# Kernel tuning notes

Hardware: AMD Instinct MI355X
Metric: run time of the kernel (lower is better)

Reference implementation:

```python
import jax, jax.numpy as jnp
import numpy as np

# WFN symmetry table: symmetry index -> (px, py, pz) angular-momentum exponents
# (s; px,py,pz; 6 cartesian d; 10 cartesian f) as in standard .wfn files.
WFN_SYMMETRY_INDEX = np.array([
    [0, 0, 0],
    [1, 0, 0], [0, 1, 0], [0, 0, 1],
    [2, 0, 0], [0, 2, 0], [0, 0, 2], [1, 1, 0], [1, 0, 1], [0, 1, 1],
    [3, 0, 0], [0, 3, 0], [0, 0, 3], [2, 1, 0], [2, 0, 1], [0, 2, 1],
    [1, 2, 0], [1, 0, 2], [0, 1, 2], [1, 1, 1],
], dtype=np.float32)


def setup_inputs() -> dict:
    key = jax.random.key(0)
    k1, k2, k3, k4, k5 = jax.random.split(key, 5)
    n, ms, na, nps = 16, 4096, 32, 512
    dv = jax.random.normal(k1, (n, ms, na, 3), jnp.float32)          # sample->atom displacement vectors
    centers = jax.random.randint(k2, (n, nps), 0, na)                # primitive -> atom index (-1 = pad)
    exp = jax.random.uniform(k3, (n, nps), jnp.float32)              # GTO exponents (>0)
    sym = jax.random.randint(k4, (n, nps), 0, 20)                    # symmetry index into WFN table
    dm = jax.random.normal(k5, (n, nps, nps), jnp.float32) / nps     # density matrices
    return {"dv": dv, "centers": centers, "exp": exp, "sym": sym, "dm": dm}


def _density(dv, exp, dm, centers, sym):
    # dv: [n,ms,na,3]; exp: [n,np]; dm: [n,np,np]; centers/sym: [n,np] int
    sym_map = jnp.asarray(WFN_SYMMETRY_INDEX)
    valid = centers >= 0                                   # padded primitives marked -1
    c = jnp.where(valid, centers, 0)
    s = jnp.where(valid, sym, 0)
    r2 = jnp.sum(dv * dv, axis=-1)                         # [n,ms,na] squared distances
    r2g = jax.vmap(lambda r, ci: r[:, ci])(r2, c)          # [n,ms,np] gather per primitive
    dvg = jax.vmap(lambda d, ci: d[:, ci])(dv, c)          # [n,ms,np,3]
    pw = sym_map[s]                                        # [n,np,3] angular exponents
    # GTO kernel: dx^px * dy^py * dz^pz * exp(-alpha * r^2)
    ang = jnp.prod(jnp.power(dvg, pw[:, None, :, :]), axis=-1)   # [n,ms,np]
    basis = ang * jnp.exp(-exp[:, None, :] * r2g)
    basis = basis * valid[:, None, :].astype(basis.dtype)        # zero out padded primitives
    # rho = sum_pq basis_p * dm_pq * basis_q (per molecule, per sample point)
    return jnp.einsum('nmp,npq,nmq->nm', basis, dm, basis)


def reference(dv, centers, exp, sym, dm):
    return _density(dv, exp, dm, centers, sym)
```

## Files before the change

### kernel.cpp

```cpp
#include <hip/hip_runtime.h>
#include <stdint.h>

#define NMOL 16
#define MS   4096
#define NA   32
#define NP   512
#define BM   64
#define TBL  65536u

typedef __attribute__((ext_vector_type(4))) float  f32x4;
typedef __attribute__((ext_vector_type(4))) unsigned int u32x4;
typedef __attribute__((ext_vector_type(2))) unsigned int u32x2;
typedef __attribute__((ext_vector_type(8))) short  s16x8;
typedef unsigned int uint;
typedef unsigned short ushort;

#define WS_DMF_OFF   0u
#define WS_DMF_SZ    (16u*512u*512u*2u)
#define WS_M2A_OFF   (WS_DMF_OFF + WS_DMF_SZ)
#define WS_M2A_SZ    (16u*512u*4u)
#define WS_M2B_OFF   (WS_M2A_OFF + WS_M2A_SZ)
#define WS_M2B_SZ    (16u*512u*4u)
#define WS_ALPH_OFF  (WS_M2B_OFF + WS_M2B_SZ)

__device__ __constant__ uint c_pw[20] = {
  0x000,
  0x001, 0x010, 0x100,
  0x002, 0x020, 0x200, 0x011, 0x101, 0x110,
  0x003, 0x030, 0x300, 0x012, 0x102, 0x120, 0x021, 0x201, 0x210, 0x111
};

__device__ __forceinline__ ushort f2bf(float f) {
  uint u = __float_as_uint(f);
  u = u + 0x7fffu + ((u >> 16) & 1u);
  return (ushort)(u >> 16);
}
__device__ __forceinline__ float bflo(uint u) { return __uint_as_float(u << 16); }
__device__ __forceinline__ float bfhi(uint u) { return __uint_as_float(u & 0xFFFF0000u); }
__device__ __forceinline__ float cvt16lo(uint u) {
  float r; asm("v_cvt_f32_f16 %0, %1" : "=v"(r) : "v"(u)); return r;
}
__device__ __forceinline__ float cvt16hi(uint u) {
  uint s = u >> 16; float r; asm("v_cvt_f32_f16 %0, %1" : "=v"(r) : "v"(s)); return r;
}
__device__ __forceinline__ uint pkmul(uint a, uint b) {
  uint r; asm("v_pk_mul_f16 %0, %1, %2" : "=v"(r) : "v"(a), "v"(b)); return r;
}
__device__ __forceinline__ s16x8 mkfrag(u32x2 lo, u32x2 hi) {
  union { uint u[4]; s16x8 v; } x;
  x.u[0] = lo[0]; x.u[1] = lo[1]; x.u[2] = hi[0]; x.u[3] = hi[1];
  return x.v;
}

__global__ void dm_pack(const float* __restrict__ dm, short* __restrict__ dmF,
                        const int* __restrict__ centers, const int* __restrict__ sym,
                        const float* __restrict__ expg,
                        uint* __restrict__ m2a, uint* __restrict__ m2b,
                        float* __restrict__ alphaS) {
  __shared__ float tile[NP * 16];
  __shared__ float tileT[16 * (NP + 2)];
  const int Q = blockIdx.x, n = blockIdx.y;
  const int t = threadIdx.x;
  const float* base = dm + (size_t)n * NP * NP;
  const float* src  = base + Q * 16;
#pragma unroll
  for (int i = 0; i < 32; ++i) {
    int e = t + 256 * i;
    int p = e >> 4, c = e & 15;
    tile[e] = src[(size_t)p * NP + c];
  }
  const float* srcT = base + (size_t)(Q * 16) * NP;
#pragma unroll
  for (int i = 0; i < 32; ++i) {
    int e = t + 256 * i;
    tileT[(e >> 9) * (NP + 2) + (e & 511)] = srcT[e];
  }
  if (n == 0) {
    int i = Q * 256 + t;
    int craw = centers[i], s = sym[i];
    bool valid = (craw >= 0);
    uint c = (uint)((valid ? craw : 0) & (NA - 1));
    int si = valid ? s : 0;
    si = (si >= 0 && si < 20) ? si : 0;
    uint pw = c_pw[si];
    uint d = (pw & 15u) + ((pw >> 4) & 15u) + ((pw >> 8) & 15u);
    uint h[3]; int k = 0;
#pragma unroll
    for (uint ax = 0; ax < 3; ++ax) {
      uint e = (pw >> (4 * ax)) & 15u;
      for (uint r = 0; r < e; ++r) if (k < 3) h[k++] = c * 512u + ax * 128u;
    }
    while (k < 3) h[k++] = c * 512u;
    m2a[i] = h[0] | (h[1] << 16);
    m2b[i] = h[2] | (d << 14) | (c << 16);
    alphaS[i] = (valid ? -expg[i] : -1e5f) * 1.44269504088896f;
  }
  __syncthreads();
  short* dst = dmF + ((size_t)(n * 32 + Q) * 16) * 512;
#pragma unroll
  for (int i = 0; i < 4; ++i) {
    int v = t + 256 * i;
    int kblk = v >> 6, l = v & 63;
    int p0 = kblk * 32 + ((l >> 4) << 3);
    int col = l & 15;
    int q = Q * 16 + col;
    s16x8 o;
#pragma unroll
    for (int j = 0; j < 8; ++j) {
      int p = p0 + j;
      float w = 0.0f;
      if (p < q)       w = tile[p * 16 + col] + tileT[col * (NP + 2) + p];
      else if (p == q) w = tile[p * 16 + col];
      o[j] = (short)f2bf(w);
    }
    *(s16x8*)(dst + (size_t)v * 8) = o;
  }
}

__launch_bounds__(512, 4)
__global__ void wfn_fused8(const float* __restrict__ dv,
                           const uint* __restrict__ m2aG,
                           const uint* __restrict__ m2bG,
                           const float* __restrict__ alG,
                           const short* __restrict__ dmF,
                           float* __restrict__ out) {
  __shared__ __align__(16) char smem[81920];
  const int t = threadIdx.x;
  const int bid = ((blockIdx.x & 7) << 7) + (blockIdx.x >> 3);
  const int n  = bid >> 6;
  const int m0 = (bid & 63) * BM;

  {
    const float* dvg = dv + (size_t)(n * MS + m0) * (NA * 3);
#pragma unroll
    for (int k = 0; k < 4; ++k) {
      int idx = t + 512 * k;
      int m = idx >> 5, c = idx & 31;
      const float* p = dvg + (m * NA + c) * 3;
      float x = p[0], y = p[1], z = p[2];
      float r2 = fmaf(x, x, fmaf(y, y, z * z));
      uint base = TBL + (uint)c * 512u
                + ((uint)((m >> 3) ^ (c & 7)) << 4) + (uint)((m & 7) << 1);
      *(_Float16*)(smem + base)       = (_Float16)x;
      *(_Float16*)(smem + base + 128) = (_Float16)y;
      *(_Float16*)(smem + base + 256) = (_Float16)z;
      *(_Float16*)(smem + base + 384) = (_Float16)r2;
    }
  }
  __syncthreads();

  {
    const int p = t;
    const uint ma = m2aG[n * NP + p], mb = m2bG[n * NP + p];
    const float al = alG[n * NP + p];
    const uint h0 = ma & 0xFFFFu, h1 = ma >> 16;
    const uint h2 = mb & 0x3FFFu;
    const uint d  = (mb >> 14) & 3u;
    const uint cs = (h0 >> 9) & 7u;
    const uint rh = (h0 & 0xFE00u) + 384u;
    const bool ge2 = (d >= 2), eq3 = (d == 3), eq0 = (d == 0);
    const uint wbase = ((uint)(p >> 5) << 10) + (((uint)(p >> 2) & 1u) << 9)
                     + ((((uint)p & 31u) >> 3) << 7) + (((uint)p & 3u) << 5);
#pragma unroll
    for (int j = 0; j < 8; ++j) {
      uint off = (uint)((j ^ (int)cs) << 4);
      u32x4 qr = *(const u32x4*)(smem + TBL + rh + off);
      u32x4 q0, q1, q2;
      if (!eq0) q0 = *(const u32x4*)(smem + TBL + h0 + off);
      if (ge2)  q1 = *(const u32x4*)(smem + TBL + h1 + off);
      if (eq3)  q2 = *(const u32x4*)(smem + TBL + h2 + off);
      uint res[4];
#pragma unroll
      for (int w = 0; w < 4; ++w) {
        uint m_ = eq0 ? 0x3C003C00u : q0[w];
        if (ge2) m_ = pkmul(m_, q1[w]);
        if (eq3) m_ = pkmul(m_, q2[w]);
        float r2l = cvt16lo(qr[w]), r2h = cvt16hi(qr[w]);
        float a0 = al * r2l, a1 = al * r2h;
        float e0, e1;
        asm("v_exp_f32 %0, %1" : "=v"(e0) : "v"(a0));
        asm("v_exp_f32 %0, %1" : "=v"(e1) : "v"(a1));
        float v0 = cvt16lo(m_) * e0, v1 = cvt16hi(m_) * e1;
        asm("v_cvt_pk_bf16_f32 %0, %1, %2" : "=v"(res[w]) : "v"(v0), "v"(v1));
      }
      *(u32x4*)(smem + wbase + ((uint)(j >> 1) << 14) + ((uint)(j & 1) << 4))
          = *(u32x4*)res;
    }
  }
  __syncthreads();

  const int lane = t & 63, wv = t >> 6, li = lane & 15, kg = lane >> 4;
  const uint lane8 = (uint)lane << 3;
  const short* dmFn = dmF + (size_t)n * (32 * 16 * 512);

  f32x4 acc[4][4];
#pragma unroll
  for (int rf = 0; rf < 4; ++rf)
#pragma unroll
    for (int qf = 0; qf < 4; ++qf)
      acc[rf][qf] = (f32x4){0.f, 0.f, 0.f, 0.f};

  const short* bp0 = dmFn + ((size_t)((wv)      * 16) * 512) + lane * 8;
  const short* bp1 = dmFn + ((size_t)((wv + 8)  * 16) * 512) + lane * 8;
  const short* bp2 = dmFn + ((size_t)((wv + 16) * 16) * 512) + lane * 8;
  const short* bp3 = dmFn + ((size_t)((wv + 24) * 16) * 512) + lane * 8;
  const int kq0 = wv >> 1, kq1 = (wv + 8) >> 1, kq2 = (wv + 16) >> 1;
  const int kmaxw = (wv + 24) >> 1;

  for (int kblk = 0; kblk <= kmaxw; ++kblk) {
    uint ak = lane8 + ((uint)kblk << 10);
    u32x2 l0, g0, l1, g1, l2, g2, l3, g3;
    asm volatile("ds_read_b64_tr_b16 %0, %1 offset:0"     : "=v"(l0) : "v"(ak));
    asm volatile("ds_read_b64_tr_b16 %0, %1 offset:512"   : "=v"(g0) : "v"(ak));
    asm volatile("ds_read_b64_tr_b16 %0, %1 offset:16384" : "=v"(l1) : "v"(ak));
    asm volatile("ds_read_b64_tr_b16 %0, %1 offset:16896" : "=v"(g1) : "v"(ak));
    asm volatile("ds_read_b64_tr_b16 %0, %1 offset:32768" : "=v"(l2) : "v"(ak));
    asm volatile("ds_read_b64_tr_b16 %0, %1 offset:33280" : "=v"(g2) : "v"(ak));
    asm volatile("ds_read_b64_tr_b16 %0, %1 offset:49152" : "=v"(l3) : "v"(ak));
    asm volatile("ds_read_b64_tr_b16 %0, %1 offset:49664" : "=v"(g3) : "v"(ak));
    s16x8 bf0, bf1, bf2, bf3;
    if (kblk <= kq0) bf0 = *(const s16x8*)(bp0 + kblk * 512);
    if (kblk <= kq1) bf1 = *(const s16x8*)(bp1 + kblk * 512);
    if (kblk <= kq2) bf2 = *(const s16x8*)(bp2 + kblk * 512);
    bf3 = *(const s16x8*)(bp3 + kblk * 512);
    asm volatile("s_waitcnt lgkmcnt(0)");
    __builtin_amdgcn_sched_barrier(0);
    s16x8 af[4];
    af[0] = mkfrag(l0, g0); af[1] = mkfrag(l1, g1);
    af[2] = mkfrag(l2, g2); af[3] = mkfrag(l3, g3);
    __builtin_amdgcn_s_setprio(1);
    if (kblk <= kq0) {
#pragma unroll
      for (int rf = 0; rf < 4; ++rf)
        acc[rf][0] = __builtin_amdgcn_mfma_f32_16x16x32_bf16(af[rf], bf0, acc[rf][0], 0, 0, 0);
    }
    if (kblk <= kq1) {
#pragma unroll
      for (int rf = 0; rf < 4; ++rf)
        acc[rf][1] = __builtin_amdgcn_mfma_f32_16x16x32_bf16(af[rf], bf1, acc[rf][1], 0, 0, 0);
    }
    if (kblk <= kq2) {
#pragma unroll
      for (int rf = 0; rf < 4; ++rf)
        acc[rf][2] = __builtin_amdgcn_mfma_f32_16x16x32_bf16(af[rf], bf2, acc[rf][2], 0, 0, 0);
    }
#pragma unroll
    for (int rf = 0; rf < 4; ++rf)
      acc[rf][3] = __builtin_amdgcn_mfma_f32_16x16x32_bf16(af[rf], bf3, acc[rf][3], 0, 0, 0);
    __builtin_amdgcn_s_setprio(0);
  }

  float part[16];
#pragma unroll
  for (int x = 0; x < 16; ++x) part[x] = 0.0f;
  uint qp[4];
#pragma unroll
  for (int qf = 0; qf < 4; ++qf) {
    int q = (wv + 8 * qf) * 16 + li;
    qp[qf] = ((uint)(q >> 5) << 10) + (((uint)(q >> 2) & 1u) << 9)
           + (((uint)(q & 31) >> 3) << 7) + ((uint)(q & 3) << 5) + ((uint)kg << 3);
  }
#pragma unroll
  for (int rf = 0; rf < 4; ++rf) {
#pragma unroll
    for (int qf = 0; qf < 4; ++qf) {
      u32x2 dq = *(const u32x2*)(smem + ((uint)rf << 14) + qp[qf]);
      part[rf * 4 + 0] = fmaf(acc[rf][qf][0], bflo(dq[0]), part[rf * 4 + 0]);
      part[rf * 4 + 1] = fmaf(acc[rf][qf][1], bfhi(dq[0]), part[rf * 4 + 1]);
      part[rf * 4 + 2] = fmaf(acc[rf][qf][2], bflo(dq[1]), part[rf * 4 + 2]);
      part[rf * 4 + 3] = fmaf(acc[rf][qf][3], bfhi(dq[1]), part[rf * 4 + 3]);
    }
  }

  __syncthreads();
#pragma unroll
  for (int x = 0; x < 16; ++x) {
    float v = part[x];
    v += __shfl_xor(v, 1);
    v += __shfl_xor(v, 2);
    v += __shfl_xor(v, 4);
    v += __shfl_xor(v, 8);
    part[x] = v;
  }
  float* rbuf = (float*)smem;
  if (li == 0) {
#pragma unroll
    for (int rf = 0; rf < 4; ++rf)
#pragma unroll
      for (int jj = 0; jj < 4; ++jj)
        rbuf[wv * 64 + rf * 16 + kg * 4 + jj] = part[rf * 4 + jj];
  }
  __syncthreads();
  if (t < BM) {
    float s = 0.0f;
#pragma unroll
    for (int w = 0; w < 8; ++w) s += rbuf[w * 64 + t];
    out[(size_t)n * MS + m0 + t] = s;
  }
}

extern "C" void kernel_launch(void* const* d_in, const int* in_sizes, int n_in,
                              void* d_out, int out_size, void* d_ws, size_t ws_size,
                              hipStream_t stream) {
  const float* dv      = (const float*)d_in[0];
  const int*   centers = (const int*)d_in[1];
  const float* expg    = (const float*)d_in[2];
  const int*   sym     = (const int*)d_in[3];
  const float* dm      = (const float*)d_in[4];
  float* out = (float*)d_out;

  char* ws = (char*)d_ws;
  short* dmF    = (short*)(ws + WS_DMF_OFF);
  uint*  m2a    = (uint*)(ws + WS_M2A_OFF);
  uint*  m2b    = (uint*)(ws + WS_M2B_OFF);
  float* alphaS = (float*)(ws + WS_ALPH_OFF);

  dm_pack<<<dim3(32, NMOL), 256, 0, stream>>>(dm, dmF, centers, sym, expg,
                                              m2a, m2b, alphaS);
  wfn_fused8<<<dim3(NMOL * (MS / BM)), 512, 0, stream>>>(dv, m2a, m2b, alphaS, dmF, out);
}
```

Before: 51.92 us.

## Interleave basis computation in chunks with MFMA k-loop; rework dm_pack tiling

The basis evaluation is split into four 128-primitive chunks. Only the first chunk is computed before the GEMM, and each later chunk is computed while the transposed LDS reads for the current k-block are in flight. This lets exp/convert ALU work overlap with the MFMA loop instead of running as a separate serial phase, at the cost of extra barriers between chunks. dm_pack also changes to 32-column tiles with a padded single tile, reading the transpose half directly from global memory with vector loads, and launches half as many blocks.

```diff
diff --git a/kernel.cpp b/kernel.cpp
--- a/kernel.cpp
+++ b/kernel.cpp
@@ -57,65 +57,135 @@
                         const float* __restrict__ expg,
                         uint* __restrict__ m2a, uint* __restrict__ m2b,
                         float* __restrict__ alphaS) {
-  __shared__ float tile[NP * 16];
-  __shared__ float tileT[16 * (NP + 2)];
-  const int Q = blockIdx.x, n = blockIdx.y;
+  __shared__ float tile[NP * 33];
+  const int Qp = blockIdx.x, n = blockIdx.y;
   const int t = threadIdx.x;
   const float* base = dm + (size_t)n * NP * NP;
-  const float* src  = base + Q * 16;
-#pragma unroll
-  for (int i = 0; i < 32; ++i) {
+  const float* src  = base + Qp * 32;
+#pragma unroll
+  for (int i = 0; i < 64; ++i) {
     int e = t + 256 * i;
-    int p = e >> 4, c = e & 15;
-    tile[e] = src[(size_t)p * NP + c];
-  }
-  const float* srcT = base + (size_t)(Q * 16) * NP;
-#pragma unroll
-  for (int i = 0; i < 32; ++i) {
-    int e = t + 256 * i;
-    tileT[(e >> 9) * (NP + 2) + (e & 511)] = srcT[e];
+    int p = e >> 5, c = e & 31;
+    tile[p * 33 + c] = src[(size_t)p * NP + c];
   }
   if (n == 0) {
-    int i = Q * 256 + t;
-    int craw = centers[i], s = sym[i];
-    bool valid = (craw >= 0);
-    uint c = (uint)((valid ? craw : 0) & (NA - 1));
-    int si = valid ? s : 0;
-    si = (si >= 0 && si < 20) ? si : 0;
-    uint pw = c_pw[si];
-    uint d = (pw & 15u) + ((pw >> 4) & 15u) + ((pw >> 8) & 15u);
-    uint h[3]; int k = 0;
-#pragma unroll
-    for (uint ax = 0; ax < 3; ++ax) {
-      uint e = (pw >> (4 * ax)) & 15u;
-      for (uint r = 0; r < e; ++r) if (k < 3) h[k++] = c * 512u + ax * 128u;
-    }
-    while (k < 3) h[k++] = c * 512u;
-    m2a[i] = h[0] | (h[1] << 16);
-    m2b[i] = h[2] | (d << 14) | (c << 16);
-    alphaS[i] = (valid ? -expg[i] : -1e5f) * 1.44269504088896f;
-  }
-  __syncthreads();
-  short* dst = dmF + ((size_t)(n * 32 + Q) * 16) * 512;
-#pragma unroll
-  for (int i = 0; i < 4; ++i) {
-    int v = t + 256 * i;
-    int kblk = v >> 6, l = v & 63;
+#pragma unroll
+    for (int kk = 0; kk < 2; ++kk) {
+      int i = Qp * 512 + t + 256 * kk;
+      int craw = centers[i], s = sym[i];
+      bool valid = (craw >= 0);
+      uint c = (uint)((valid ? craw : 0) & (NA - 1));
+      int si = valid ? s : 0;
+      si = (si >= 0 && si < 20) ? si : 0;
+      uint pw = c_pw[si];
+      uint d = (pw & 15u) + ((pw >> 4) & 15u) + ((pw >> 8) & 15u);
+      uint h[3]; int k = 0;
+#pragma unroll
+      for (uint ax = 0; ax < 3; ++ax) {
+        uint e2 = (pw >> (4 * ax)) & 15u;
+        for (uint r = 0; r < e2; ++r) if (k < 3) h[k++] = c * 512u + ax * 128u;
+      }
+      while (k < 3) h[k++] = c * 512u;
+      m2a[i] = h[0] | (h[1] << 16);
+      m2b[i] = h[2] | (d << 14) | (c << 16);
+      alphaS[i] = (valid ? -expg[i] : -1e5f) * 1.44269504088896f;
+    }
+  }
+  __syncthreads();
+#pragma unroll
+  for (int it = 0; it < 8; ++it) {
+    int v = t + 256 * it;
+    int qq = v >> 10, vv = v & 1023;
+    int kblk = vv >> 6, l = vv & 63;
     int p0 = kblk * 32 + ((l >> 4) << 3);
     int col = l & 15;
-    int q = Q * 16 + col;
+    int q = (Qp * 2 + qq) * 16 + col;
+    f32x4 r0 = *(const f32x4*)(base + (size_t)q * NP + p0);
+    f32x4 r1 = *(const f32x4*)(base + (size_t)q * NP + p0 + 4);
     s16x8 o;
 #pragma unroll
     for (int j = 0; j < 8; ++j) {
       int p = p0 + j;
-      float w = 0.0f;
-      if (p < q)       w = tile[p * 16 + col] + tileT[col * (NP + 2) + p];
-      else if (p == q) w = tile[p * 16 + col];
+      float tpq = tile[p * 33 + qq * 16 + col];
+      float rv = (j < 4) ? r0[j] : r1[j - 4];
+      float w = (p < q) ? (tpq + rv) : ((p == q) ? tpq : 0.0f);
       o[j] = (short)f2bf(w);
     }
-    *(s16x8*)(dst + (size_t)v * 8) = o;
-  }
-}
+    short* dst = dmF + ((size_t)(n * 32 + Qp * 2 + qq) * 16) * 512;
+    *(s16x8*)(dst + (size_t)vv * 8) = o;
+  }
+}
+
+__device__ __forceinline__ void basis_slice(char* smem, uint ma, uint mb, float al,
+                                            int p, int jb) {
+  uint h0 = ma & 0xFFFFu, h1 = ma >> 16, h2 = mb & 0x3FFFu;
+  uint d  = (mb >> 14) & 3u;
+  uint cs = (h0 >> 9) & 7u;
+  uint rh = (h0 & 0xFE00u) + 384u;
+  const bool ge2 = (d >= 2), eq3 = (d == 3), eq0 = (d == 0);
+  uint wbase = (((uint)p >> 5) << 10) + ((((uint)p >> 2) & 1u) << 9)
+             + ((((uint)p & 31u) >> 3) << 7) + (((uint)p & 3u) << 5);
+#pragma unroll
+  for (int jo = 0; jo < 2; ++jo) {
+    int j = jb + jo;
+    uint off = (uint)((j ^ (int)cs) << 4);
+    u32x4 qr = *(const u32x4*)(smem + TBL + rh + off);
+    u32x4 q0, q1, q2;
+    if (!eq0) q0 = *(const u32x4*)(smem + TBL + h0 + off);
+    if (ge2)  q1 = *(const u32x4*)(smem + TBL + h1 + off);
+    if (eq3)  q2 = *(const u32x4*)(smem + TBL + h2 + off);
+    uint res[4];
+#pragma unroll
+    for (int w = 0; w < 4; ++w) {
+      uint m_ = eq0 ? 0x3C003C00u : q0[w];
+      if (ge2) m_ = pkmul(m_, q1[w]);
+      if (eq3) m_ = pkmul(m_, q2[w]);
+      float r2l = cvt16lo(qr[w]), r2h = cvt16hi(qr[w]);
+      float a0 = al * r2l, a1 = al * r2h;
+      float e0, e1;
+      asm("v_exp_f32 %0, %1" : "=v"(e0) : "v"(a0));
+      asm("v_exp_f32 %0, %1" : "=v"(e1) : "v"(a1));
+      float v0 = cvt16lo(m_) * e0, v1 = cvt16hi(m_) * e1;
+      asm("v_cvt_pk_bf16_f32 %0, %1, %2" : "=v"(res[w]) : "v"(v0), "v"(v1));
+    }
+    *(u32x4*)(smem + wbase + ((uint)(j >> 1) << 14) + ((uint)(j & 1) << 4)) = *(u32x4*)res;
+  }
+}
+
+#define MFMA16(a, b, c) __builtin_amdgcn_mfma_f32_16x16x32_bf16(a, b, c, 0, 0, 0)
+
+#define ISSUE_TR(AK) \
+  asm volatile("ds_read_b64_tr_b16 %0, %1 offset:0"     : "=v"(l0) : "v"(AK)); \
+  asm volatile("ds_read_b64_tr_b16 %0, %1 offset:512"   : "=v"(g0) : "v"(AK)); \
+  asm volatile("ds_read_b64_tr_b16 %0, %1 offset:16384" : "=v"(l1) : "v"(AK)); \
+  asm volatile("ds_read_b64_tr_b16 %0, %1 offset:16896" : "=v"(g1) : "v"(AK)); \
+  asm volatile("ds_read_b64_tr_b16 %0, %1 offset:32768" : "=v"(l2) : "v"(AK)); \
+  asm volatile("ds_read_b64_tr_b16 %0, %1 offset:33280" : "=v"(g2) : "v"(AK)); \
+  asm volatile("ds_read_b64_tr_b16 %0, %1 offset:49152" : "=v"(l3) : "v"(AK)); \
+  asm volatile("ds_read_b64_tr_b16 %0, %1 offset:49664" : "=v"(g3) : "v"(AK));
+
+#define FINISH_TRIP(KBLK) do { \
+  s16x8 bf0, bf1, bf2, bf3; \
+  const bool c0 = (KBLK) <= kq0, c1 = (KBLK) <= kq1, c2 = (KBLK) <= kq2; \
+  if (c0) bf0 = *(const s16x8*)(bp0 + (KBLK) * 512); \
+  if (c1) bf1 = *(const s16x8*)(bp1 + (KBLK) * 512); \
+  if (c2) bf2 = *(const s16x8*)(bp2 + (KBLK) * 512); \
+  bf3 = *(const s16x8*)(bp3 + (KBLK) * 512); \
+  asm volatile("s_waitcnt lgkmcnt(0)"); \
+  __builtin_amdgcn_sched_barrier(0); \
+  s16x8 af0 = mkfrag(l0, g0), af1 = mkfrag(l1, g1); \
+  s16x8 af2 = mkfrag(l2, g2), af3 = mkfrag(l3, g3); \
+  __builtin_amdgcn_s_setprio(1); \
+  if (c0) { acc[0][0]=MFMA16(af0,bf0,acc[0][0]); acc[1][0]=MFMA16(af1,bf0,acc[1][0]); \
+            acc[2][0]=MFMA16(af2,bf0,acc[2][0]); acc[3][0]=MFMA16(af3,bf0,acc[3][0]); } \
+  if (c1) { acc[0][1]=MFMA16(af0,bf1,acc[0][1]); acc[1][1]=MFMA16(af1,bf1,acc[1][1]); \
+            acc[2][1]=MFMA16(af2,bf1,acc[2][1]); acc[3][1]=MFMA16(af3,bf1,acc[3][1]); } \
+  if (c2) { acc[0][2]=MFMA16(af0,bf2,acc[0][2]); acc[1][2]=MFMA16(af1,bf2,acc[1][2]); \
+            acc[2][2]=MFMA16(af2,bf2,acc[2][2]); acc[3][2]=MFMA16(af3,bf2,acc[3][2]); } \
+  acc[0][3]=MFMA16(af0,bf3,acc[0][3]); acc[1][3]=MFMA16(af1,bf3,acc[1][3]); \
+  acc[2][3]=MFMA16(af2,bf3,acc[2][3]); acc[3][3]=MFMA16(af3,bf3,acc[3][3]); \
+  __builtin_amdgcn_s_setprio(0); \
+} while (0)
 
 __launch_bounds__(512, 4)
 __global__ void wfn_fused8(const float* __restrict__ dv,
@@ -149,43 +219,14 @@
   }
   __syncthreads();
 
+  const int pl = t & 127;
+  const int jb = (t >> 7) * 2;
+  const int mbase = n * NP;
+  uint cma, cmb; float cal;
   {
-    const int p = t;
-    const uint ma = m2aG[n * NP + p], mb = m2bG[n * NP + p];
-    const float al = alG[n * NP + p];
-    const uint h0 = ma & 0xFFFFu, h1 = ma >> 16;
-    const uint h2 = mb & 0x3FFFu;
-    const uint d  = (mb >> 14) & 3u;
-    const uint cs = (h0 >> 9) & 7u;
-    const uint rh = (h0 & 0xFE00u) + 384u;
-    const bool ge2 = (d >= 2), eq3 = (d == 3), eq0 = (d == 0);
-    const uint wbase = ((uint)(p >> 5) << 10) + (((uint)(p >> 2) & 1u) << 9)
-                     + ((((uint)p & 31u) >> 3) << 7) + (((uint)p & 3u) << 5);
-#pragma unroll
-    for (int j = 0; j < 8; ++j) {
-      uint off = (uint)((j ^ (int)cs) << 4);
-      u32x4 qr = *(const u32x4*)(smem + TBL + rh + off);
-      u32x4 q0, q1, q2;
-      if (!eq0) q0 = *(const u32x4*)(smem + TBL + h0 + off);
-      if (ge2)  q1 = *(const u32x4*)(smem + TBL + h1 + off);
-      if (eq3)  q2 = *(const u32x4*)(smem + TBL + h2 + off);
-      uint res[4];
-#pragma unroll
-      for (int w = 0; w < 4; ++w) {
-        uint m_ = eq0 ? 0x3C003C00u : q0[w];
-        if (ge2) m_ = pkmul(m_, q1[w]);
-        if (eq3) m_ = pkmul(m_, q2[w]);
-        float r2l = cvt16lo(qr[w]), r2h = cvt16hi(qr[w]);
-        float a0 = al * r2l, a1 = al * r2h;
-        float e0, e1;
-        asm("v_exp_f32 %0, %1" : "=v"(e0) : "v"(a0));
-        asm("v_exp_f32 %0, %1" : "=v"(e1) : "v"(a1));
-        float v0 = cvt16lo(m_) * e0, v1 = cvt16hi(m_) * e1;
-        asm("v_cvt_pk_bf16_f32 %0, %1, %2" : "=v"(res[w]) : "v"(v0), "v"(v1));
-      }
-      *(u32x4*)(smem + wbase + ((uint)(j >> 1) << 14) + ((uint)(j & 1) << 4))
-          = *(u32x4*)res;
-    }
+    cma = m2aG[mbase + 128 + pl]; cmb = m2bG[mbase + 128 + pl]; cal = alG[mbase + 128 + pl];
+    uint a0 = m2aG[mbase + pl];  uint b0 = m2bG[mbase + pl];  float l0_ = alG[mbase + pl];
+    basis_slice(smem, a0, b0, l0_, pl, jb);
   }
   __syncthreads();
 
@@ -207,47 +248,31 @@
   const int kq0 = wv >> 1, kq1 = (wv + 8) >> 1, kq2 = (wv + 16) >> 1;
   const int kmaxw = (wv + 24) >> 1;
 
-  for (int kblk = 0; kblk <= kmaxw; ++kblk) {
-    uint ak = lane8 + ((uint)kblk << 10);
-    u32x2 l0, g0, l1, g1, l2, g2, l3, g3;
-    asm volatile("ds_read_b64_tr_b16 %0, %1 offset:0"     : "=v"(l0) : "v"(ak));
-    asm volatile("ds_read_b64_tr_b16 %0, %1 offset:512"   : "=v"(g0) : "v"(ak));
-    asm volatile("ds_read_b64_tr_b16 %0, %1 offset:16384" : "=v"(l1) : "v"(ak));
-    asm volatile("ds_read_b64_tr_b16 %0, %1 offset:16896" : "=v"(g1) : "v"(ak));
-    asm volatile("ds_read_b64_tr_b16 %0, %1 offset:32768" : "=v"(l2) : "v"(ak));
-    asm volatile("ds_read_b64_tr_b16 %0, %1 offset:33280" : "=v"(g2) : "v"(ak));
-    asm volatile("ds_read_b64_tr_b16 %0, %1 offset:49152" : "=v"(l3) : "v"(ak));
-    asm volatile("ds_read_b64_tr_b16 %0, %1 offset:49664" : "=v"(g3) : "v"(ak));
-    s16x8 bf0, bf1, bf2, bf3;
-    if (kblk <= kq0) bf0 = *(const s16x8*)(bp0 + kblk * 512);
-    if (kblk <= kq1) bf1 = *(const s16x8*)(bp1 + kblk * 512);
-    if (kblk <= kq2) bf2 = *(const s16x8*)(bp2 + kblk * 512);
-    bf3 = *(const s16x8*)(bp3 + kblk * 512);
-    asm volatile("s_waitcnt lgkmcnt(0)");
-    __builtin_amdgcn_sched_barrier(0);
-    s16x8 af[4];
-    af[0] = mkfrag(l0, g0); af[1] = mkfrag(l1, g1);
-    af[2] = mkfrag(l2, g2); af[3] = mkfrag(l3, g3);
-    __builtin_amdgcn_s_setprio(1);
-    if (kblk <= kq0) {
-#pragma unroll
-      for (int rf = 0; rf < 4; ++rf)
-        acc[rf][0] = __builtin_amdgcn_mfma_f32_16x16x32_bf16(af[rf], bf0, acc[rf][0], 0, 0, 0);
-    }
-    if (kblk <= kq1) {
-#pragma unroll
-      for (int rf = 0; rf < 4; ++rf)
-        acc[rf][1] = __builtin_amdgcn_mfma_f32_16x16x32_bf16(af[rf], bf1, acc[rf][1], 0, 0, 0);
-    }
-    if (kblk <= kq2) {
-#pragma unroll
-      for (int rf = 0; rf < 4; ++rf)
-        acc[rf][2] = __builtin_amdgcn_mfma_f32_16x16x32_bf16(af[rf], bf2, acc[rf][2], 0, 0, 0);
-    }
-#pragma unroll
-    for (int rf = 0; rf < 4; ++rf)
-      acc[rf][3] = __builtin_amdgcn_mfma_f32_16x16x32_bf16(af[rf], bf3, acc[rf][3], 0, 0, 0);
-    __builtin_amdgcn_s_setprio(0);
+  for (int cnk = 0; cnk < 4; ++cnk) {
+    const int kbeg = cnk * 4;
+    const int kend = (cnk < 3) ? (kbeg + 3) : kmaxw;
+    {
+      uint ak = lane8 + ((uint)kbeg << 10);
+      u32x2 l0, g0, l1, g1, l2, g2, l3, g3;
+      ISSUE_TR(ak);
+      if (cnk < 3) {
+        uint nma = 0u, nmb = 0u; float nal = 0.f;
+        if (cnk < 2) {
+          int mp = mbase + (cnk + 2) * 128 + pl;
+          nma = m2aG[mp]; nmb = m2bG[mp]; nal = alG[mp];
+        }
+        basis_slice(smem, cma, cmb, cal, (cnk + 1) * 128 + pl, jb);
+        cma = nma; cmb = nmb; cal = nal;
+      }
+      FINISH_TRIP(kbeg);
+    }
+    for (int kblk = kbeg + 1; kblk <= kend; ++kblk) {
+      uint ak = lane8 + ((uint)kblk << 10);
+      u32x2 l0, g0, l1, g1, l2, g2, l3, g3;
+      ISSUE_TR(ak);
+      FINISH_TRIP(kblk);
+    }
+    if (cnk < 3) __syncthreads();
   }
 
   float part[16];
@@ -315,7 +340,7 @@
   uint*  m2b    = (uint*)(ws + WS_M2B_OFF);
   float* alphaS = (float*)(ws + WS_ALPH_OFF);
 
-  dm_pack<<<dim3(32, NMOL), 256, 0, stream>>>(dm, dmF, centers, sym, expg,
+  dm_pack<<<dim3(16, NMOL), 256, 0, stream>>>(dm, dmF, centers, sym, expg,
                                               m2a, m2b, alphaS);
   wfn_fused8<<<dim3(NMOL * (MS / BM)), 512, 0, stream>>>(dv, m2a, m2b, alphaS, dmF, out);
 }
```

Measured after the change: 57.41 us. 10.6% more time.
